# Performance work log

Measured on AMD Instinct MI355X. Metric: run time of the kernel, lower is better.

## Reference

```python
import jax, jax.numpy as jnp
import numpy as np

N_NODES = 100000
N_EDGES = 1600000
DK = 32
OUT_DIM = 32


def setup_inputs() -> dict:
    key = jax.random.key(0)
    ks = jax.random.split(key, 7)
    X = jax.random.normal(ks[0], (N_NODES, DK), dtype=jnp.float32)
    K = jax.random.normal(ks[1], (N_NODES, DK), dtype=jnp.float32)
    V = jax.random.normal(ks[2], (N_NODES, DK), dtype=jnp.float32)
    # output projection (nn.Dense(out_dim)) params
    W_o = jax.random.normal(ks[3], (DK, OUT_DIM), dtype=jnp.float32) / np.sqrt(DK)
    b_o = jnp.zeros((OUT_DIM,), dtype=jnp.float32)
    # sparsity descriptor td: edge list, dst sorted so segment ops see sorted ids
    src = jax.random.randint(ks[4], (N_EDGES,), 0, N_NODES, dtype=jnp.int32)
    dst = jnp.sort(jax.random.randint(ks[5], (N_EDGES,), 0, N_NODES, dtype=jnp.int32))
    return {"X": X, "K": K, "V": V, "W_o": W_o, "b_o": b_o,
            "src": src, "dst": dst, "num_seg": N_NODES}


def reference(X, K, V, W_o, b_o, src, dst, num_seg):
    dk = X.shape[-1]
    # per-edge attention logits: <Q[dst], K[src]> / dk  -> (E,)
    scores = jnp.einsum('ed,ed->e', jnp.take(X, dst, axis=0),
                        jnp.take(K, src, axis=0)) / dk
    # segment (per-neighborhood) softmax over edges sharing a dst node
    seg_max = jax.ops.segment_max(scores, dst, num_segments=num_seg,
                                  indices_are_sorted=True)
    e = jnp.exp(scores - jnp.take(seg_max, dst))
    denom = jax.ops.segment_sum(e, dst, num_segments=num_seg,
                                indices_are_sorted=True)
    alpha = e / jnp.take(denom, dst)  # (E,)
    # weighted aggregation of values, scattered back to nodes -> (N, dk)
    agg = jax.ops.segment_sum(alpha[:, None] * jnp.take(V, src, axis=0), dst,
                              num_segments=num_seg, indices_are_sorted=True)
    # output projection W_o
    return agg @ W_o + b_o
```

## Files before the change

kernel.cpp:

```cpp
#include <hip/hip_runtime.h>
#include <math.h>

#define DK 32
#define OUT_DIM 32

typedef float    f32x4 __attribute__((ext_vector_type(4)));
typedef _Float16 h2    __attribute__((ext_vector_type(2)));
typedef _Float16 h8    __attribute__((ext_vector_type(8)));

#if __has_builtin(__builtin_amdgcn_fdot2)
#define FDOT2(a, b, c) __builtin_amdgcn_fdot2((a), (b), (c), false)
#else
#define FDOT2(a, b, c) ((c) + (float)(a).x * (float)(b).x + (float)(a).y * (float)(b).y)
#endif

__device__ __forceinline__ h2 as_h2(unsigned u) {
    union { unsigned u; h2 h; } v; v.u = u; return v.h;
}
__device__ __forceinline__ unsigned as_u32(h2 h) {
    union { unsigned u; h2 h; } v; v.h = h; return v.u;
}
__device__ __forceinline__ h2 shfl_xor_h2(h2 v, int m) {
    union { unsigned u; h2 h; } x; x.h = v;
    x.u = (unsigned)__shfl_xor((int)x.u, m);
    return x.h;
}

__global__ void prep_kernel(const int* __restrict__ dst,
                            const float* __restrict__ K,
                            const float* __restrict__ V,
                            int E, int N,
                            int* __restrict__ row_ptr,
                            unsigned* __restrict__ KVH) {
    const int t = blockIdx.x * blockDim.x + threadIdx.x;
    if (t < E) {
        const int cur  = dst[t];
        const int prev = (t == 0) ? -1 : dst[t - 1];
        for (int j = prev + 1; j <= cur; ++j) row_ptr[j] = t;
        if (t == E - 1) {
            for (int j = cur + 1; j <= N; ++j) row_ptr[j] = E;
        }
    }
    if (t < N * DK) {
        const int s = t >> 5;
        const int r = t & 31;
        const int c = r >> 2;
        const int q = r & 3;
        const float* srcp = (q < 2) ? K : V;
        const int d0 = c * 4 + (q & 1) * 2;
        h2 h;
        h.x = (_Float16)srcp[s * DK + d0];
        h.y = (_Float16)srcp[s * DK + d0 + 1];
        KVH[t] = as_u32(h);
    }
}

__global__ void build_row_ptr_kernel(const int* __restrict__ dst, int E, int N,
                                     int* __restrict__ row_ptr) {
    int e = blockIdx.x * blockDim.x + threadIdx.x;
    if (e >= E) return;
    int cur  = dst[e];
    int prev = (e == 0) ? -1 : dst[e - 1];
    for (int j = prev + 1; j <= cur; ++j) row_ptr[j] = e;
    if (e == E - 1) {
        for (int j = cur + 1; j <= N; ++j) row_ptr[j] = E;
    }
}

__global__ __launch_bounds__(256) void gat_fused_kernel(
    const float* __restrict__ X, const uint4* __restrict__ KV,
    const float* __restrict__ Wo, const float* __restrict__ bo,
    const int* __restrict__ src, const int* __restrict__ row_ptr,
    float* __restrict__ out, int N) {

    __shared__ uint4 s_part[16 * 17];

    const int tid  = threadIdx.x;
    const int w    = tid >> 6;
    const int lane = tid & 63;
    const int g    = lane >> 3;
    const int c    = lane & 7;

    const int n_blk = blockIdx.x * 16;
    const int n_w   = n_blk + w * 4;

    const int rpv = row_ptr[min(n_w + min(lane, 4), N)];

    const float4* X4 = (const float4*)X;
    unsigned* part32 = (unsigned*)s_part;
    const float scale = 0.03125f;

    for (int pr = 0; pr < 2; ++pr) {
        const int ia = pr * 2;
        const int beginA = __builtin_amdgcn_readlane(rpv, ia);
        const int endA   = __builtin_amdgcn_readlane(rpv, ia + 1);
        const int endB   = __builtin_amdgcn_readlane(rpv, ia + 2);
        const int beginB = endA;
        const int nA = n_w + ia;
        const int nB = nA + 1;

        float4 qa = X4[min(nA, N - 1) * 8 + c];
        float4 qb = X4[min(nB, N - 1) * 8 + c];
        h2 qa01, qa23, qb01, qb23;
        qa01.x = (_Float16)(qa.x * scale);  qa01.y = (_Float16)(qa.y * scale);
        qa23.x = (_Float16)(qa.z * scale);  qa23.y = (_Float16)(qa.w * scale);
        qb01.x = (_Float16)(qb.x * scale);  qb01.y = (_Float16)(qb.y * scale);
        qb23.x = (_Float16)(qb.z * scale);  qb23.y = (_Float16)(qb.w * scale);

        float lA = 0.0f, lB = 0.0f;
        h2 aA01 = (h2)0, aA23 = (h2)0, aB01 = (h2)0, aB23 = (h2)0;

        const int capA = max(endA - 1, 0);
        const int capB = max(endB - 1, 0);
        int eA = beginA, eB = beginB;

        while (eA < endA || eB < endB) {
            const int sa0 = src[min(eA + g,     capA)];
            const int sa1 = src[min(eA + 8 + g, capA)];
            const int sb0 = src[min(eB + g,     capB)];
            const int sb1 = src[min(eB + 8 + g, capB)];
            const uint4 A0 = KV[sa0 * 8 + c];
            const uint4 A1 = KV[sa1 * 8 + c];
            const uint4 B0 = KV[sb0 * 8 + c];
            const uint4 B1 = KV[sb1 * 8 + c];

            float p0 = FDOT2(as_h2(A0.y), qa23, FDOT2(as_h2(A0.x), qa01, 0.0f));
            float p1 = FDOT2(as_h2(A1.y), qa23, FDOT2(as_h2(A1.x), qa01, 0.0f));
            float p2 = FDOT2(as_h2(B0.y), qb23, FDOT2(as_h2(B0.x), qb01, 0.0f));
            float p3 = FDOT2(as_h2(B1.y), qb23, FDOT2(as_h2(B1.x), qb01, 0.0f));
            p0 += __shfl_xor(p0, 1);  p1 += __shfl_xor(p1, 1);
            p2 += __shfl_xor(p2, 1);  p3 += __shfl_xor(p3, 1);
            p0 += __shfl_xor(p0, 2);  p1 += __shfl_xor(p1, 2);
            p2 += __shfl_xor(p2, 2);  p3 += __shfl_xor(p3, 2);
            p0 += __shfl_xor(p0, 4);  p1 += __shfl_xor(p1, 4);
            p2 += __shfl_xor(p2, 4);  p3 += __shfl_xor(p3, 4);

            const float w0 = (eA + g     < endA) ? __expf(p0) : 0.0f;
            const float w1 = (eA + 8 + g < endA) ? __expf(p1) : 0.0f;
            const float w2 = (eB + g     < endB) ? __expf(p2) : 0.0f;
            const float w3 = (eB + 8 + g < endB) ? __expf(p3) : 0.0f;
            lA += w0 + w1;
            lB += w2 + w3;

            h2 wh0; wh0.x = (_Float16)w0; wh0.y = wh0.x;
            h2 wh1; wh1.x = (_Float16)w1; wh1.y = wh1.x;
            h2 wh2; wh2.x = (_Float16)w2; wh2.y = wh2.x;
            h2 wh3; wh3.x = (_Float16)w3; wh3.y = wh3.x;
            aA01 += wh0 * as_h2(A0.z);  aA23 += wh0 * as_h2(A0.w);
            aA01 += wh1 * as_h2(A1.z);  aA23 += wh1 * as_h2(A1.w);
            aB01 += wh2 * as_h2(B0.z);  aB23 += wh2 * as_h2(B0.w);
            aB01 += wh3 * as_h2(B1.z);  aB23 += wh3 * as_h2(B1.w);

            eA += 16; eB += 16;
        }

        lA   += __shfl_xor(lA, 8);
        aA01 += shfl_xor_h2(aA01, 8);
        aA23 += shfl_xor_h2(aA23, 8);
        lA += __shfl_xor(lA, 16);  lA += __shfl_xor(lA, 32);

        lB   += __shfl_xor(lB, 8);
        aB01 += shfl_xor_h2(aB01, 8);
        aB23 += shfl_xor_h2(aB23, 8);
        lB += __shfl_xor(lB, 16);  lB += __shfl_xor(lB, 32);

        const float invA = (endA > beginA) ? (1.0f / lA) : 0.0f;
        const float invB = (endB > beginB) ? (1.0f / lB) : 0.0f;
        h2 ivA; ivA.x = (_Float16)invA; ivA.y = ivA.x;
        h2 ivB; ivB.x = (_Float16)invB; ivB.y = ivB.x;
        aA01 *= ivA;  aA23 *= ivA;
        aB01 *= ivB;  aB23 *= ivB;

        if ((g & 1) == 0) {
            const int p   = g >> 1;
            const int row = w * 4 + ia;
            int off = row * 68 + p * 16 + c * 2;
            part32[off]     = as_u32(aA01);
            part32[off + 1] = as_u32(aA23);
            off += 68;
            part32[off]     = as_u32(aB01);
            part32[off + 1] = as_u32(aB23);
        }
    }

    __syncthreads();

    if (w == 0) {
        const int quad = lane >> 4;
        const int col  = lane & 15;

        union BF { h8 v; _Float16 u[8]; };
        BF bf0, bf1;
#pragma unroll
        for (int j2 = 0; j2 < 8; ++j2) {
            bf0.u[j2] = (_Float16)Wo[(quad * 8 + j2) * OUT_DIM + col];
            bf1.u[j2] = (_Float16)Wo[(quad * 8 + j2) * OUT_DIM + 16 + col];
        }
        const float bias0 = bo[col];
        const float bias1 = bo[16 + col];

        union AF { uint4 u; h8 v; };
        f32x4 C0 = {bias0, bias0, bias0, bias0};
        f32x4 C1 = {bias1, bias1, bias1, bias1};
#pragma unroll
        for (int cc = 0; cc < 4; ++cc) {
            AF a;
            a.u = s_part[col * 17 + cc * 4 + quad];
            C0 = __builtin_amdgcn_mfma_f32_16x16x32_f16(a.v, bf0.v, C0, 0, 0, 0);
            C1 = __builtin_amdgcn_mfma_f32_16x16x32_f16(a.v, bf1.v, C1, 0, 0, 0);
        }
#pragma unroll
        for (int r = 0; r < 4; ++r) {
            const int n = n_blk + quad * 4 + r;
            if (n < N) {
                out[n * OUT_DIM + col]      = C0[r];
                out[n * OUT_DIM + 16 + col] = C1[r];
            }
        }
    }
}

__global__ __launch_bounds__(256) void gat_node_f32_kernel(
    const float* __restrict__ X, const float* __restrict__ Km,
    const float* __restrict__ Vm, const float* __restrict__ Wo,
    const float* __restrict__ bo, const int* __restrict__ src,
    const int* __restrict__ row_ptr, float* __restrict__ out, int N) {
    const int tid  = threadIdx.x;
    const int wave = tid >> 6;
    const int lane = tid & 63;
    const int g    = lane >> 3;
    const int c    = lane & 7;
    const int j    = lane & 31;
    const int half = lane >> 5;
    const int n = blockIdx.x * 4 + wave;
    if (n >= N) return;
    const int begin = row_ptr[n];
    const int end   = row_ptr[n + 1];
    const float4* X4 = (const float4*)X;
    const float4* K4 = (const float4*)Km;
    const float4* V4 = (const float4*)Vm;
    const float4 q4 = X4[n * 8 + c];
    float  l   = 0.0f;
    float4 acc = make_float4(0.0f, 0.0f, 0.0f, 0.0f);
    for (int e0 = begin; e0 < end; e0 += 16) {
        const int  ea = e0 + g;
        const int  eb = ea + 8;
        const bool va = ea < end;
        const bool vb = eb < end;
        const int sa = src[min(ea, end - 1)];
        const int sb = src[min(eb, end - 1)];
        const float4 ka  = K4[sa * 8 + c];
        const float4 kb  = K4[sb * 8 + c];
        const float4 vva = V4[sa * 8 + c];
        const float4 vvb = V4[sb * 8 + c];
        float pa = fmaf(ka.x, q4.x, fmaf(ka.y, q4.y, fmaf(ka.z, q4.z, ka.w * q4.w)));
        float pb = fmaf(kb.x, q4.x, fmaf(kb.y, q4.y, fmaf(kb.z, q4.z, kb.w * q4.w)));
        pa += __shfl_xor(pa, 1);  pb += __shfl_xor(pb, 1);
        pa += __shfl_xor(pa, 2);  pb += __shfl_xor(pb, 2);
        pa += __shfl_xor(pa, 4);  pb += __shfl_xor(pb, 4);
        const float wa = va ? __expf(pa * 0.03125f) : 0.0f;
        const float wb = vb ? __expf(pb * 0.03125f) : 0.0f;
        l += wa + wb;
        acc.x = fmaf(wa, vva.x, acc.x);  acc.y = fmaf(wa, vva.y, acc.y);
        acc.z = fmaf(wa, vva.z, acc.z);  acc.w = fmaf(wa, vva.w, acc.w);
        acc.x = fmaf(wb, vvb.x, acc.x);  acc.y = fmaf(wb, vvb.y, acc.y);
        acc.z = fmaf(wb, vvb.z, acc.z);  acc.w = fmaf(wb, vvb.w, acc.w);
    }
#pragma unroll
    for (int m = 8; m <= 32; m <<= 1) {
        l     += __shfl_xor(l, m);
        acc.x += __shfl_xor(acc.x, m);
        acc.y += __shfl_xor(acc.y, m);
        acc.z += __shfl_xor(acc.z, m);
        acc.w += __shfl_xor(acc.w, m);
    }
    const float inv = (end > begin) ? (1.0f / l) : 0.0f;
    float ag[4] = {acc.x, acc.y, acc.z, acc.w};
    float s = 0.0f;
#pragma unroll
    for (int k = 0; k < 32; ++k) {
        const float a = __int_as_float(
            __builtin_amdgcn_readlane(__float_as_int(ag[k & 3]), k >> 2));
        s = fmaf(a, Wo[k * OUT_DIM + j], s);
    }
    if (half == 0) {
        out[n * OUT_DIM + j] = fmaf(s, inv, bo[j]);
    }
}

extern "C" void kernel_launch(void* const* d_in, const int* in_sizes, int n_in,
                              void* d_out, int out_size, void* d_ws, size_t ws_size,
                              hipStream_t stream) {
    const float* X  = (const float*)d_in[0];
    const float* Km = (const float*)d_in[1];
    const float* Vm = (const float*)d_in[2];
    const float* Wo = (const float*)d_in[3];
    const float* bo = (const float*)d_in[4];
    const int* src  = (const int*)d_in[5];
    const int* dst  = (const int*)d_in[6];

    const int N = in_sizes[0] / DK;
    const int E = in_sizes[5];

    int* row_ptr = (int*)d_ws;
    const size_t kv_off = (((size_t)(N + 1) * 4) + 127) & ~(size_t)127;
    unsigned* KV = (unsigned*)((char*)d_ws + kv_off);
    const size_t need = kv_off + (size_t)N * DK * 4;
    float* out = (float*)d_out;

    const int tb = 256;

    if (ws_size >= need) {
        const int total  = N * DK;
        const int prep_n = (E > total) ? E : total;
        prep_kernel<<<(prep_n + tb - 1) / tb, tb, 0, stream>>>(dst, Km, Vm, E, N,
                                                               row_ptr, KV);
        const int grid = (N + 15) / 16;
        gat_fused_kernel<<<grid, 256, 0, stream>>>(X, (const uint4*)KV, Wo, bo,
                                                   src, row_ptr, out, N);
    } else {
        build_row_ptr_kernel<<<(E + tb - 1) / tb, tb, 0, stream>>>(dst, E, N, row_ptr);
        const int grid = (N + 3) / 4;
        gat_node_f32_kernel<<<grid, 256, 0, stream>>>(X, Km, Vm, Wo, bo,
                                                      src, row_ptr, out, N);
    }
}
```

Measured before the change: 134.0 us.

## Software-pipeline edge gathers in fused GAT kernel and vectorize KV prep

The edge loop now uses a double-buffered software pipeline. It prefetches the next chunk's KV rows and the src indices two chunks ahead while computing on the current chunk, to hide the latency of the dependent src-then-KV loads. The prep kernel now packs K and V to fp16 one float4 per thread instead of one scalar pair per thread, with the same output layout. The pipeline raises register pressure, which may lower occupancy, and it makes the loop control more complex.

```diff
diff --git a/kernel.cpp b/kernel.cpp
--- a/kernel.cpp
+++ b/kernel.cpp
@@ -27,11 +27,11 @@
 }
 
 __global__ void prep_kernel(const int* __restrict__ dst,
-                            const float* __restrict__ K,
-                            const float* __restrict__ V,
+                            const float4* __restrict__ K4,
+                            const float4* __restrict__ V4,
                             int E, int N,
                             int* __restrict__ row_ptr,
-                            unsigned* __restrict__ KVH) {
+                            uint4* __restrict__ KVH) {
     const int t = blockIdx.x * blockDim.x + threadIdx.x;
     if (t < E) {
         const int cur  = dst[t];
@@ -41,17 +41,17 @@
             for (int j = cur + 1; j <= N; ++j) row_ptr[j] = E;
         }
     }
-    if (t < N * DK) {
-        const int s = t >> 5;
-        const int r = t & 31;
-        const int c = r >> 2;
-        const int q = r & 3;
-        const float* srcp = (q < 2) ? K : V;
-        const int d0 = c * 4 + (q & 1) * 2;
-        h2 h;
-        h.x = (_Float16)srcp[s * DK + d0];
-        h.y = (_Float16)srcp[s * DK + d0 + 1];
-        KVH[t] = as_u32(h);
+    if (t < N * 8) {
+        const float4 kf = K4[t];
+        const float4 vf = V4[t];
+        h2 k01, k23, v01, v23;
+        k01.x = (_Float16)kf.x;  k01.y = (_Float16)kf.y;
+        k23.x = (_Float16)kf.z;  k23.y = (_Float16)kf.w;
+        v01.x = (_Float16)vf.x;  v01.y = (_Float16)vf.y;
+        v23.x = (_Float16)vf.z;  v23.y = (_Float16)vf.w;
+        uint4 o;
+        o.x = as_u32(k01); o.y = as_u32(k23); o.z = as_u32(v01); o.w = as_u32(v23);
+        KVH[t] = o;
     }
 }
 
@@ -114,16 +114,8 @@
         const int capB = max(endB - 1, 0);
         int eA = beginA, eB = beginB;
 
-        while (eA < endA || eB < endB) {
-            const int sa0 = src[min(eA + g,     capA)];
-            const int sa1 = src[min(eA + 8 + g, capA)];
-            const int sb0 = src[min(eB + g,     capB)];
-            const int sb1 = src[min(eB + 8 + g, capB)];
-            const uint4 A0 = KV[sa0 * 8 + c];
-            const uint4 A1 = KV[sa1 * 8 + c];
-            const uint4 B0 = KV[sb0 * 8 + c];
-            const uint4 B1 = KV[sb1 * 8 + c];
-
+        auto step = [&](const uint4& A0, const uint4& A1,
+                        const uint4& B0, const uint4& B1) {
             float p0 = FDOT2(as_h2(A0.y), qa23, FDOT2(as_h2(A0.x), qa01, 0.0f));
             float p1 = FDOT2(as_h2(A1.y), qa23, FDOT2(as_h2(A1.x), qa01, 0.0f));
             float p2 = FDOT2(as_h2(B0.y), qb23, FDOT2(as_h2(B0.x), qb01, 0.0f));
@@ -150,8 +142,64 @@
             aA01 += wh1 * as_h2(A1.z);  aA23 += wh1 * as_h2(A1.w);
             aB01 += wh2 * as_h2(B0.z);  aB23 += wh2 * as_h2(B0.w);
             aB01 += wh3 * as_h2(B1.z);  aB23 += wh3 * as_h2(B1.w);
-
-            eA += 16; eB += 16;
+        };
+
+        if (eA < endA || eB < endB) {
+            int sp0 = src[min(eA + g,     capA)];
+            int sp1 = src[min(eA + 8 + g, capA)];
+            int sp2 = src[min(eB + g,     capB)];
+            int sp3 = src[min(eB + 8 + g, capB)];
+            uint4 P0 = KV[sp0 * 8 + c];
+            uint4 P1 = KV[sp1 * 8 + c];
+            uint4 P2 = KV[sp2 * 8 + c];
+            uint4 P3 = KV[sp3 * 8 + c];
+            int sq0 = 0, sq1 = 0, sq2 = 0, sq3 = 0;
+            uint4 Q0, Q1, Q2, Q3;
+            bool more = (eA + 16 < endA) || (eB + 16 < endB);
+            if (more) {
+                sq0 = src[min(eA + 16 + g, capA)];
+                sq1 = src[min(eA + 24 + g, capA)];
+                sq2 = src[min(eB + 16 + g, capB)];
+                sq3 = src[min(eB + 24 + g, capB)];
+            }
+            for (;;) {
+                bool more2 = false;
+                if (more) {
+                    Q0 = KV[sq0 * 8 + c];
+                    Q1 = KV[sq1 * 8 + c];
+                    Q2 = KV[sq2 * 8 + c];
+                    Q3 = KV[sq3 * 8 + c];
+                    more2 = (eA + 32 < endA) || (eB + 32 < endB);
+                    if (more2) {
+                        sp0 = src[min(eA + 32 + g, capA)];
+                        sp1 = src[min(eA + 40 + g, capA)];
+                        sp2 = src[min(eB + 32 + g, capB)];
+                        sp3 = src[min(eB + 40 + g, capB)];
+                    }
+                }
+                step(P0, P1, P2, P3);
+                eA += 16; eB += 16;
+                if (!more) break;
+
+                bool more3 = false;
+                if (more2) {
+                    P0 = KV[sp0 * 8 + c];
+                    P1 = KV[sp1 * 8 + c];
+                    P2 = KV[sp2 * 8 + c];
+                    P3 = KV[sp3 * 8 + c];
+                    more3 = (eA + 32 < endA) || (eB + 32 < endB);
+                    if (more3) {
+                        sq0 = src[min(eA + 32 + g, capA)];
+                        sq1 = src[min(eA + 40 + g, capA)];
+                        sq2 = src[min(eB + 32 + g, capB)];
+                        sq3 = src[min(eB + 40 + g, capB)];
+                    }
+                }
+                step(Q0, Q1, Q2, Q3);
+                eA += 16; eB += 16;
+                if (!more2) break;
+                more = more3;
+            }
         }
 
         lA   += __shfl_xor(lA, 8);
@@ -311,10 +359,11 @@
     const int tb = 256;
 
     if (ws_size >= need) {
-        const int total  = N * DK;
+        const int total  = N * 8;
         const int prep_n = (E > total) ? E : total;
-        prep_kernel<<<(prep_n + tb - 1) / tb, tb, 0, stream>>>(dst, Km, Vm, E, N,
-                                                               row_ptr, KV);
+        prep_kernel<<<(prep_n + tb - 1) / tb, tb, 0, stream>>>(
+            dst, (const float4*)Km, (const float4*)Vm, E, N,
+            row_ptr, (uint4*)KV);
         const int grid = (N + 15) / 16;
         gat_fused_kernel<<<grid, 256, 0, stream>>>(X, (const uint4*)KV, Wo, bo,
                                                    src, row_ptr, out, N);
```

New measurement: 133.1 us. No clear change (-0.6%).
